# Kernel tuning notes

Measured on AMD Instinct MI355X. Metric: run time of the kernel, lower is better.

Reference implementation:

```python
import jax, jax.numpy as jnp
import numpy as np

N = 262144          # number of samples
D = 512             # embedding dim
NUM_IDS = 8192      # label vocabulary size (fixed segment count for jit)


def setup_inputs() -> dict:
    key = jax.random.key(0)
    k_emb, k_lab = jax.random.split(key)
    emb = jax.random.normal(k_emb, (N, D), dtype=jnp.float32)
    labels = jax.random.randint(k_lab, (N,), 0, NUM_IDS, dtype=jnp.int64)
    return {"emb": emb, "labels": labels}


def reference(emb, labels):
    # torch.unique(labels, return_inverse=True); fixed size for jit.
    uniq_ids, inv = jnp.unique(labels, return_inverse=True, size=NUM_IDS, fill_value=-1)
    # scatter_add_ of rows grouped by inverse index -> segmented sum
    summed = jax.ops.segment_sum(emb, inv, num_segments=NUM_IDS)   # [NUM_IDS, D]
    # bincount(inv, minlength=num_ids)
    counts = jnp.bincount(inv, length=NUM_IDS)                      # [NUM_IDS]
    agg = summed / jnp.maximum(counts, 1).astype(emb.dtype)[:, None]
    return (agg, uniq_ids)
```

## Files before the change

### kernel.cpp

```cpp
#include <hip/hip_runtime.h>

#define NUM_IDS 8192
#define D 512


__global__ __launch_bounds__(256) void k_zero(int* __restrict__ cnt) {
    int i = blockIdx.x * 256 + threadIdx.x;
    if (i < NUM_IDS) cnt[i] = 0;
}

__global__ __launch_bounds__(256) void k_count(const int* __restrict__ labels, int n4,
                                               int* __restrict__ cnt,
                                               int* __restrict__ pos) {
    int i = blockIdx.x * 256 + threadIdx.x;
    if (i < n4) {
        int4 l = reinterpret_cast<const int4*>(labels)[i];
        int4 p;
        p.x = atomicAdd(&cnt[l.x], 1);
        p.y = atomicAdd(&cnt[l.y], 1);
        p.z = atomicAdd(&cnt[l.z], 1);
        p.w = atomicAdd(&cnt[l.w], 1);
        reinterpret_cast<int4*>(pos)[i] = p;
    }
}

__global__ __launch_bounds__(1024) void k_scan(const int* __restrict__ cnt,
                                               int* __restrict__ rank,
                                               int* __restrict__ offs,
                                               int* __restrict__ nuniq,
                                               float* __restrict__ uniq_out) {
    __shared__ int s_f[16], s_c[16];
    __shared__ int s_total;
    int t = threadIdx.x;
    int lane = t & 63, wave = t >> 6;
    int c[8], f[8];
    int fs = 0, cs = 0;
    int base = t * 8;
    int4 c0 = reinterpret_cast<const int4*>(cnt)[t * 2];
    int4 c1 = reinterpret_cast<const int4*>(cnt)[t * 2 + 1];
    c[0] = c0.x; c[1] = c0.y; c[2] = c0.z; c[3] = c0.w;
    c[4] = c1.x; c[5] = c1.y; c[6] = c1.z; c[7] = c1.w;
#pragma unroll
    for (int j = 0; j < 8; ++j) {
        f[j] = (c[j] > 0) ? 1 : 0;
        fs += f[j]; cs += c[j];
    }
    int fi = fs, ci = cs;
#pragma unroll
    for (int d = 1; d < 64; d <<= 1) {
        int fo = __shfl_up(fi, d, 64);
        int co = __shfl_up(ci, d, 64);
        if (lane >= d) { fi += fo; ci += co; }
    }
    if (lane == 63) { s_f[wave] = fi; s_c[wave] = ci; }
    __syncthreads();
    if (t == 0) {
        int af = 0, ac = 0;
#pragma unroll
        for (int w = 0; w < 16; ++w) {
            int tf = s_f[w], tc = s_c[w];
            s_f[w] = af; s_c[w] = ac;
            af += tf; ac += tc;
        }
        s_total = af;
        nuniq[0] = af;
    }
    __syncthreads();
    int fexcl = (fi - fs) + s_f[wave];
    int cexcl = (ci - cs) + s_c[wave];
    int total = s_total;
#pragma unroll
    for (int j = 0; j < 8; ++j) {
        int id = base + j;
        rank[id] = fexcl;
        offs[id] = cexcl;
        if (f[j]) uniq_out[fexcl] = (float)id;
        if (id >= total) uniq_out[id] = -1.0f;
        fexcl += f[j];
        cexcl += c[j];
    }
}

__global__ __launch_bounds__(256) void k_fill(const int* __restrict__ labels, int n4,
                                              const int* __restrict__ offs,
                                              const int* __restrict__ pos,
                                              int* __restrict__ rowidx) {
    int i = blockIdx.x * 256 + threadIdx.x;
    if (i < n4) {
        int4 l = reinterpret_cast<const int4*>(labels)[i];
        int4 p = reinterpret_cast<const int4*>(pos)[i];
        int b = i * 4;
        rowidx[offs[l.x] + p.x] = b + 0;
        rowidx[offs[l.y] + p.y] = b + 1;
        rowidx[offs[l.z] + p.z] = b + 2;
        rowidx[offs[l.w] + p.w] = b + 3;
    }
}

__global__ __launch_bounds__(128) void k_agg(const float* __restrict__ emb,
                                             const int* __restrict__ cnt,
                                             const int* __restrict__ rank,
                                             const int* __restrict__ offs,
                                             const int* __restrict__ rowidx,
                                             const int* __restrict__ nuniq,
                                             float* __restrict__ agg) {
    int id = blockIdx.x;
    int t = threadIdx.x;
    int n = cnt[id];
    const float4* eb = reinterpret_cast<const float4*>(emb);

    if (n == 0) {
        int outrow = nuniq[0] + (id - rank[id]);
        float4 z = {0.f, 0.f, 0.f, 0.f};
        reinterpret_cast<float4*>(agg + (size_t)outrow * D)[t] = z;
        return;
    }
    int off = offs[id];
    float4 a0 = {0,0,0,0}, a1 = {0,0,0,0}, a2 = {0,0,0,0}, a3 = {0,0,0,0};
    int r = 0;
    for (; r + 4 <= n; r += 4) {
        int r0 = rowidx[off + r + 0];
        int r1 = rowidx[off + r + 1];
        int r2 = rowidx[off + r + 2];
        int r3 = rowidx[off + r + 3];
        float4 v0 = eb[(size_t)r0 * (D / 4) + t];
        float4 v1 = eb[(size_t)r1 * (D / 4) + t];
        float4 v2 = eb[(size_t)r2 * (D / 4) + t];
        float4 v3 = eb[(size_t)r3 * (D / 4) + t];
        a0.x += v0.x; a0.y += v0.y; a0.z += v0.z; a0.w += v0.w;
        a1.x += v1.x; a1.y += v1.y; a1.z += v1.z; a1.w += v1.w;
        a2.x += v2.x; a2.y += v2.y; a2.z += v2.z; a2.w += v2.w;
        a3.x += v3.x; a3.y += v3.y; a3.z += v3.z; a3.w += v3.w;
    }
    for (; r < n; ++r) {
        int r0 = rowidx[off + r];
        float4 v0 = eb[(size_t)r0 * (D / 4) + t];
        a0.x += v0.x; a0.y += v0.y; a0.z += v0.z; a0.w += v0.w;
    }
    float inv = 1.0f / (float)n;
    float4 o;
    o.x = ((a0.x + a1.x) + (a2.x + a3.x)) * inv;
    o.y = ((a0.y + a1.y) + (a2.y + a3.y)) * inv;
    o.z = ((a0.z + a1.z) + (a2.z + a3.z)) * inv;
    o.w = ((a0.w + a1.w) + (a2.w + a3.w)) * inv;
    reinterpret_cast<float4*>(agg + (size_t)rank[id] * D)[t] = o;
}


extern "C" void kernel_launch(void* const* d_in, const int* in_sizes, int n_in,
                              void* d_out, int out_size, void* d_ws, size_t ws_size,
                              hipStream_t stream) {
    const float* emb   = (const float*)d_in[0];
    const int* labels  = (const int*)d_in[1];
    const int n  = in_sizes[1];
    const int n4 = n / 4;

    float* agg  = (float*)d_out;
    float* uniq = agg + (size_t)NUM_IDS * D;

    int* ws     = (int*)d_ws;
    int* cnt    = ws;
    int* rank   = cnt + NUM_IDS;
    int* offs   = rank + NUM_IDS;
    int* nuniq  = offs + NUM_IDS;
    int* pos    = nuniq + 64;
    int* rowidx = pos + n;

    k_zero <<<NUM_IDS / 256, 256, 0, stream>>>(cnt);
    k_count<<<(n4 + 255) / 256, 256, 0, stream>>>(labels, n4, cnt, pos);
    k_scan <<<1, 1024, 0, stream>>>(cnt, rank, offs, nuniq, uniq);
    k_fill <<<(n4 + 255) / 256, 256, 0, stream>>>(labels, n4, offs, pos, rowidx);
    k_agg  <<<NUM_IDS, 128, 0, stream>>>(emb, cnt, rank, offs, rowidx, nuniq, agg);
}
```

Measured before the change: 146.7 us.

## Fuse scan into fill kernel with redundant per-block scan; nontemporal agg loads

```diff
diff --git a/kernel.cpp b/kernel.cpp
--- a/kernel.cpp
+++ b/kernel.cpp
@@ -3,11 +3,8 @@
 #define NUM_IDS 8192
 #define D 512
 
+typedef float vfloat4 __attribute__((ext_vector_type(4)));
 
-__global__ __launch_bounds__(256) void k_zero(int* __restrict__ cnt) {
-    int i = blockIdx.x * 256 + threadIdx.x;
-    if (i < NUM_IDS) cnt[i] = 0;
-}
 
 __global__ __launch_bounds__(256) void k_count(const int* __restrict__ labels, int n4,
                                                int* __restrict__ cnt,
@@ -24,26 +21,34 @@
     }
 }
 
-__global__ __launch_bounds__(1024) void k_scan(const int* __restrict__ cnt,
-                                               int* __restrict__ rank,
-                                               int* __restrict__ offs,
-                                               int* __restrict__ nuniq,
-                                               float* __restrict__ uniq_out) {
-    __shared__ int s_f[16], s_c[16];
-    __shared__ int s_total;
+__global__ __launch_bounds__(256) void k_fill_scan(
+    const int* __restrict__ labels, int n4,
+    const int* __restrict__ cnt,
+    const int* __restrict__ pos,
+    int* __restrict__ rowidx,
+    int* __restrict__ rank,
+    int* __restrict__ offs,
+    int* __restrict__ nuniq,
+    float* __restrict__ uniq_out)
+{
+    __shared__ int s_offs[NUM_IDS];
+    __shared__ int s_f[4], s_c[4], s_total;
+
     int t = threadIdx.x;
     int lane = t & 63, wave = t >> 6;
-    int c[8], f[8];
+    int base = t * 32;
+
+    int c[32];
     int fs = 0, cs = 0;
-    int base = t * 8;
-    int4 c0 = reinterpret_cast<const int4*>(cnt)[t * 2];
-    int4 c1 = reinterpret_cast<const int4*>(cnt)[t * 2 + 1];
-    c[0] = c0.x; c[1] = c0.y; c[2] = c0.z; c[3] = c0.w;
-    c[4] = c1.x; c[5] = c1.y; c[6] = c1.z; c[7] = c1.w;
 #pragma unroll
     for (int j = 0; j < 8; ++j) {
-        f[j] = (c[j] > 0) ? 1 : 0;
-        fs += f[j]; cs += c[j];
+        int4 cc = reinterpret_cast<const int4*>(cnt)[t * 8 + j];
+        c[4 * j + 0] = cc.x; c[4 * j + 1] = cc.y;
+        c[4 * j + 2] = cc.z; c[4 * j + 3] = cc.w;
+    }
+#pragma unroll
+    for (int j = 0; j < 32; ++j) {
+        fs += (c[j] > 0); cs += c[j];
     }
     int fi = fs, ci = cs;
 #pragma unroll
@@ -57,43 +62,44 @@
     if (t == 0) {
         int af = 0, ac = 0;
 #pragma unroll
-        for (int w = 0; w < 16; ++w) {
+        for (int w = 0; w < 4; ++w) {
             int tf = s_f[w], tc = s_c[w];
             s_f[w] = af; s_c[w] = ac;
             af += tf; ac += tc;
         }
         s_total = af;
-        nuniq[0] = af;
     }
     __syncthreads();
+
     int fexcl = (fi - fs) + s_f[wave];
     int cexcl = (ci - cs) + s_c[wave];
     int total = s_total;
+    bool wr = (blockIdx.x == 0);
 #pragma unroll
-    for (int j = 0; j < 8; ++j) {
+    for (int j = 0; j < 32; ++j) {
         int id = base + j;
-        rank[id] = fexcl;
-        offs[id] = cexcl;
-        if (f[j]) uniq_out[fexcl] = (float)id;
-        if (id >= total) uniq_out[id] = -1.0f;
-        fexcl += f[j];
+        s_offs[id] = cexcl;
+        if (wr) {
+            rank[id] = fexcl;
+            offs[id] = cexcl;
+            if (c[j] > 0) uniq_out[fexcl] = (float)id;
+            if (id >= total) uniq_out[id] = -1.0f;
+        }
+        fexcl += (c[j] > 0);
         cexcl += c[j];
     }
-}
+    if (wr && t == 0) nuniq[0] = total;
+    __syncthreads();
 
-__global__ __launch_bounds__(256) void k_fill(const int* __restrict__ labels, int n4,
-                                              const int* __restrict__ offs,
-                                              const int* __restrict__ pos,
-                                              int* __restrict__ rowidx) {
-    int i = blockIdx.x * 256 + threadIdx.x;
+    int i = blockIdx.x * 256 + t;
     if (i < n4) {
         int4 l = reinterpret_cast<const int4*>(labels)[i];
         int4 p = reinterpret_cast<const int4*>(pos)[i];
         int b = i * 4;
-        rowidx[offs[l.x] + p.x] = b + 0;
-        rowidx[offs[l.y] + p.y] = b + 1;
-        rowidx[offs[l.z] + p.z] = b + 2;
-        rowidx[offs[l.w] + p.w] = b + 3;
+        rowidx[s_offs[l.x] + p.x] = b + 0;
+        rowidx[s_offs[l.y] + p.y] = b + 1;
+        rowidx[s_offs[l.z] + p.z] = b + 2;
+        rowidx[s_offs[l.w] + p.w] = b + 3;
     }
 }
 
@@ -107,43 +113,38 @@
     int id = blockIdx.x;
     int t = threadIdx.x;
     int n = cnt[id];
-    const float4* eb = reinterpret_cast<const float4*>(emb);
+    const vfloat4* eb = reinterpret_cast<const vfloat4*>(emb);
 
     if (n == 0) {
         int outrow = nuniq[0] + (id - rank[id]);
-        float4 z = {0.f, 0.f, 0.f, 0.f};
-        reinterpret_cast<float4*>(agg + (size_t)outrow * D)[t] = z;
+        vfloat4 z = {0.f, 0.f, 0.f, 0.f};
+        __builtin_nontemporal_store(z,
+            reinterpret_cast<vfloat4*>(agg + (size_t)outrow * D) + t);
         return;
     }
     int off = offs[id];
-    float4 a0 = {0,0,0,0}, a1 = {0,0,0,0}, a2 = {0,0,0,0}, a3 = {0,0,0,0};
+    vfloat4 a0 = {0,0,0,0}, a1 = {0,0,0,0}, a2 = {0,0,0,0}, a3 = {0,0,0,0};
     int r = 0;
     for (; r + 4 <= n; r += 4) {
         int r0 = rowidx[off + r + 0];
         int r1 = rowidx[off + r + 1];
         int r2 = rowidx[off + r + 2];
         int r3 = rowidx[off + r + 3];
-        float4 v0 = eb[(size_t)r0 * (D / 4) + t];
-        float4 v1 = eb[(size_t)r1 * (D / 4) + t];
-        float4 v2 = eb[(size_t)r2 * (D / 4) + t];
-        float4 v3 = eb[(size_t)r3 * (D / 4) + t];
-        a0.x += v0.x; a0.y += v0.y; a0.z += v0.z; a0.w += v0.w;
-        a1.x += v1.x; a1.y += v1.y; a1.z += v1.z; a1.w += v1.w;
-        a2.x += v2.x; a2.y += v2.y; a2.z += v2.z; a2.w += v2.w;
-        a3.x += v3.x; a3.y += v3.y; a3.z += v3.z; a3.w += v3.w;
+        vfloat4 v0 = __builtin_nontemporal_load(eb + (size_t)r0 * (D / 4) + t);
+        vfloat4 v1 = __builtin_nontemporal_load(eb + (size_t)r1 * (D / 4) + t);
+        vfloat4 v2 = __builtin_nontemporal_load(eb + (size_t)r2 * (D / 4) + t);
+        vfloat4 v3 = __builtin_nontemporal_load(eb + (size_t)r3 * (D / 4) + t);
+        a0 += v0; a1 += v1; a2 += v2; a3 += v3;
     }
     for (; r < n; ++r) {
         int r0 = rowidx[off + r];
-        float4 v0 = eb[(size_t)r0 * (D / 4) + t];
-        a0.x += v0.x; a0.y += v0.y; a0.z += v0.z; a0.w += v0.w;
+        vfloat4 v0 = __builtin_nontemporal_load(eb + (size_t)r0 * (D / 4) + t);
+        a0 += v0;
     }
     float inv = 1.0f / (float)n;
-    float4 o;
-    o.x = ((a0.x + a1.x) + (a2.x + a3.x)) * inv;
-    o.y = ((a0.y + a1.y) + (a2.y + a3.y)) * inv;
-    o.z = ((a0.z + a1.z) + (a2.z + a3.z)) * inv;
-    o.w = ((a0.w + a1.w) + (a2.w + a3.w)) * inv;
-    reinterpret_cast<float4*>(agg + (size_t)rank[id] * D)[t] = o;
+    vfloat4 o = ((a0 + a1) + (a2 + a3)) * inv;
+    __builtin_nontemporal_store(o,
+        reinterpret_cast<vfloat4*>(agg + (size_t)rank[id] * D) + t);
 }
 
 
@@ -166,9 +167,10 @@
     int* pos    = nuniq + 64;
     int* rowidx = pos + n;
 
-    k_zero <<<NUM_IDS / 256, 256, 0, stream>>>(cnt);
-    k_count<<<(n4 + 255) / 256, 256, 0, stream>>>(labels, n4, cnt, pos);
-    k_scan <<<1, 1024, 0, stream>>>(cnt, rank, offs, nuniq, uniq);
-    k_fill <<<(n4 + 255) / 256, 256, 0, stream>>>(labels, n4, offs, pos, rowidx);
-    k_agg  <<<NUM_IDS, 128, 0, stream>>>(emb, cnt, rank, offs, rowidx, nuniq, agg);
+    hipMemsetAsync(cnt, 0, NUM_IDS * sizeof(int), stream);
+
+    k_count    <<<(n4 + 255) / 256, 256, 0, stream>>>(labels, n4, cnt, pos);
+    k_fill_scan<<<(n4 + 255) / 256, 256, 0, stream>>>(labels, n4, cnt, pos, rowidx,
+                                                      rank, offs, nuniq, uniq);
+    k_agg      <<<NUM_IDS, 128, 0, stream>>>(emb, cnt, rank, offs, rowidx, nuniq, agg);
 }
```

Result: faster. 134.4 us (-8.4%).
